# Kernel tuning notes

Measured on AMD Instinct MI355X. Metric: run time of the kernel, lower is better.

The kernel has to match this reference:

```python
import jax, jax.numpy as jnp
import numpy as np

NEG_FILL = -10000000000.0

def setup_inputs() -> dict:
    key = jax.random.key(0)
    k1, k2 = jax.random.split(key)
    spans = jax.random.normal(k1, (2048, 13, 4, 1024), dtype=jnp.float32)
    attention_mask = jax.random.randint(k2, (2048, 4), 0, 2, dtype=jnp.int32)
    return {"spans": spans, "attention_mask": attention_mask}

def reference(spans, attention_mask):
    # mask: [B, S] -> broadcast to [B, 1, S, 1]; fill masked positions, then max over span dim
    mask = attention_mask[:, None, :, None] == 0
    masked = jnp.where(mask, jnp.asarray(NEG_FILL, dtype=spans.dtype), spans)
    return jnp.max(masked, axis=-2)  # [B, layers, D]
```

## Files before the change

kernel.cpp:

```cpp
#include <hip/hip_runtime.h>

#define NEG_FILL -10000000000.0f

typedef float f32x4 __attribute__((ext_vector_type(4)));

__device__ __forceinline__ f32x4 max4(f32x4 a, f32x4 b) {
    f32x4 r;
    r.x = fmaxf(a.x, b.x);
    r.y = fmaxf(a.y, b.y);
    r.z = fmaxf(a.z, b.z);
    r.w = fmaxf(a.w, b.w);
    return r;
}

__global__ __launch_bounds__(128) void MaxSpanRepr_kernel(
    const f32x4* __restrict__ spans,
    const int4* __restrict__ mask,
    f32x4* __restrict__ out) {
    const int D4 = 1024 / 4;
    int bl = blockIdx.x;
    int b  = bl / 13;
    int t  = threadIdx.x;
    int i0 = t;
    int i1 = t + 128;

    int4 mv = mask[b];

    const f32x4* base = spans + (size_t)bl * 4 * D4;

    const f32x4 nf = {NEG_FILL, NEG_FILL, NEG_FILL, NEG_FILL};
    f32x4 a0 = nf, a1 = nf, a2 = nf, a3 = nf;
    f32x4 b0 = nf, b1 = nf, b2 = nf, b3 = nf;

    if (mv.x != 0) {
        a0 = __builtin_nontemporal_load(base + 0 * D4 + i0);
        b0 = __builtin_nontemporal_load(base + 0 * D4 + i1);
    }
    if (mv.y != 0) {
        a1 = __builtin_nontemporal_load(base + 1 * D4 + i0);
        b1 = __builtin_nontemporal_load(base + 1 * D4 + i1);
    }
    if (mv.z != 0) {
        a2 = __builtin_nontemporal_load(base + 2 * D4 + i0);
        b2 = __builtin_nontemporal_load(base + 2 * D4 + i1);
    }
    if (mv.w != 0) {
        a3 = __builtin_nontemporal_load(base + 3 * D4 + i0);
        b3 = __builtin_nontemporal_load(base + 3 * D4 + i1);
    }

    f32x4 r0 = max4(max4(a0, a1), max4(a2, a3));
    f32x4 r1 = max4(max4(b0, b1), max4(b2, b3));

    f32x4* o = out + (size_t)bl * D4;
    __builtin_nontemporal_store(r0, o + i0);
    __builtin_nontemporal_store(r1, o + i1);
}

extern "C" void kernel_launch(void* const* d_in, const int* in_sizes, int n_in,
                              void* d_out, int out_size, void* d_ws, size_t ws_size,
                              hipStream_t stream) {
    const f32x4* spans = (const f32x4*)d_in[0];
    const int4* mask = (const int4*)d_in[1];
    f32x4* out = (f32x4*)d_out;

    const int B = 2048, L = 13;
    dim3 grid(B * L);
    dim3 block(128);
    MaxSpanRepr_kernel<<<grid, block, 0, stream>>>(spans, mask, out);
}
```

Measured before the change: 59.41 us.

## Assign one block per batch row and loop over layers

The grid shrinks from one 128-thread block per (batch, layer) pair to one 256-thread block per batch row. Each thread now loops over the 13 layers, unrolled by 4, reading the mask once and issuing one float4 load per span position. The aim is to cut block launch overhead and redundant mask loads. The cost is fewer blocks (2048), with less memory-level parallelism per thread in flight, which may hurt bandwidth on a memory-bound kernel.

```diff
diff --git a/kernel.cpp b/kernel.cpp
--- a/kernel.cpp
+++ b/kernel.cpp
@@ -13,48 +13,32 @@
     return r;
 }
 
-__global__ __launch_bounds__(128) void MaxSpanRepr_kernel(
+__global__ __launch_bounds__(256) void MaxSpanRepr_kernel(
     const f32x4* __restrict__ spans,
     const int4* __restrict__ mask,
     f32x4* __restrict__ out) {
     const int D4 = 1024 / 4;
-    int bl = blockIdx.x;
-    int b  = bl / 13;
-    int t  = threadIdx.x;
-    int i0 = t;
-    int i1 = t + 128;
+    int b = blockIdx.x;
+    int t = threadIdx.x;
 
     int4 mv = mask[b];
 
-    const f32x4* base = spans + (size_t)bl * 4 * D4;
+    const f32x4* sb = spans + (size_t)b * 13 * 4 * D4 + t;
+    f32x4* ob = out + (size_t)b * 13 * D4 + t;
 
     const f32x4 nf = {NEG_FILL, NEG_FILL, NEG_FILL, NEG_FILL};
-    f32x4 a0 = nf, a1 = nf, a2 = nf, a3 = nf;
-    f32x4 b0 = nf, b1 = nf, b2 = nf, b3 = nf;
 
-    if (mv.x != 0) {
-        a0 = __builtin_nontemporal_load(base + 0 * D4 + i0);
-        b0 = __builtin_nontemporal_load(base + 0 * D4 + i1);
+#pragma unroll 4
+    for (int l = 0; l < 13; ++l) {
+        const f32x4* base = sb + l * 4 * D4;
+        f32x4 a0 = nf, a1 = nf, a2 = nf, a3 = nf;
+        if (mv.x != 0) a0 = __builtin_nontemporal_load(base + 0 * D4);
+        if (mv.y != 0) a1 = __builtin_nontemporal_load(base + 1 * D4);
+        if (mv.z != 0) a2 = __builtin_nontemporal_load(base + 2 * D4);
+        if (mv.w != 0) a3 = __builtin_nontemporal_load(base + 3 * D4);
+        f32x4 r = max4(max4(a0, a1), max4(a2, a3));
+        __builtin_nontemporal_store(r, ob + l * D4);
     }
-    if (mv.y != 0) {
-        a1 = __builtin_nontemporal_load(base + 1 * D4 + i0);
-        b1 = __builtin_nontemporal_load(base + 1 * D4 + i1);
-    }
-    if (mv.z != 0) {
-        a2 = __builtin_nontemporal_load(base + 2 * D4 + i0);
-        b2 = __builtin_nontemporal_load(base + 2 * D4 + i1);
-    }
-    if (mv.w != 0) {
-        a3 = __builtin_nontemporal_load(base + 3 * D4 + i0);
-        b3 = __builtin_nontemporal_load(base + 3 * D4 + i1);
-    }
-
-    f32x4 r0 = max4(max4(a0, a1), max4(a2, a3));
-    f32x4 r1 = max4(max4(b0, b1), max4(b2, b3));
-
-    f32x4* o = out + (size_t)bl * D4;
-    __builtin_nontemporal_store(r0, o + i0);
-    __builtin_nontemporal_store(r1, o + i1);
 }
 
 extern "C" void kernel_launch(void* const* d_in, const int* in_sizes, int n_in,
@@ -64,8 +48,8 @@
     const int4* mask = (const int4*)d_in[1];
     f32x4* out = (f32x4*)d_out;
 
-    const int B = 2048, L = 13;
-    dim3 grid(B * L);
-    dim3 block(128);
+    const int B = 2048;
+    dim3 grid(B);
+    dim3 block(256);
     MaxSpanRepr_kernel<<<grid, block, 0, stream>>>(spans, mask, out);
 }
```

Measured after the change: 70.37 us. +18.5%, slower.
